# Optimization experiments

Hardware: AMD Instinct MI355X
Metric: run time of the kernel (lower is better)

Reference implementation:

```python
import jax, jax.numpy as jnp
import numpy as np

B, M, D, DE = 2, 256, 256, 64  # batch, tokens, in_dim, dep_embed_dim


def setup_inputs() -> dict:
    key = jax.random.key(0)
    ks = jax.random.split(key, 10)
    features = jax.random.normal(ks[0], (B, M + 1, D), jnp.float32)
    dep_type_adj = jax.random.normal(ks[1], (B, M, M, DE), jnp.float32)
    adj = (jax.random.uniform(ks[2], (B, M, M)) < 0.05).astype(jnp.int32)
    idx = jnp.arange(M)
    adj = adj.at[:, idx, idx].set(1)
    asp_start = jax.random.randint(ks[3], (B,), 0, 200, dtype=jnp.int32)
    asp_end = asp_start + 16
    s = lambda fan_in: 1.0 / np.sqrt(fan_in)
    Wz = jax.random.normal(ks[4], (D, D), jnp.float32) * s(D)
    bz = jax.random.normal(ks[5], (D,), jnp.float32) * s(D)
    Wa = jax.random.normal(ks[6], (D + DE + D,), jnp.float32) * s(D + DE + D)
    Wm = jax.random.normal(ks[7], (D, D + DE), jnp.float32) * s(D + DE)
    Wh = jax.random.normal(ks[8], (D, 2 * D), jnp.float32) * s(2 * D)
    return dict(features=features, dep_type_adj=dep_type_adj, deprel_adj=adj,
                asp_start=asp_start, asp_end=asp_end,
                Wz=Wz, bz=bz, Wa=Wa, Wm=Wm, Wh=Wh)


def reference(features, dep_type_adj, deprel_adj, asp_start, asp_end, Wz, bz, Wa, Wm, Wh):
    # z_linear
    zf = features @ Wz.T + bz                              # [B, M+1, D]
    f = zf[:, 1:]                                          # token feats [B, M, D]
    asp = zf[0, 1:]                                        # NOTE: original indexes features[0] (batch 0)

    # candidate neighbors for node i: out-edges (i,j) then in-edges (j,i) -> 2M slots
    dep_cat = jnp.concatenate([dep_type_adj, jnp.swapaxes(dep_type_adj, 1, 2)], axis=2)  # [B,M,2M,DE]
    mask = jnp.concatenate([deprel_adj, jnp.swapaxes(deprel_adj, 1, 2)], axis=2) != 0    # [B,M,2M]

    # attention_layer weight split over [dep | neighbor_feat | aspect_feat]
    wa_dep, wa_nf, wa_asp = Wa[:DE], Wa[DE:DE + D], Wa[DE + D:]
    s = (jnp.einsum('bike,e->bik', dep_cat, wa_dep)
         + jnp.tile(f @ wa_nf, (1, 2))[:, None, :]
         + (asp @ wa_asp)[None, :, None])                  # [B,M,2M]
    s = jnp.where(s > 0, s, 0.01 * s)                      # LeakyReLU(0.01)
    big_neg = jnp.finfo(s.dtype).min
    w = jax.nn.softmax(jnp.where(mask, s, big_neg), axis=-1)
    w = jnp.where(mask, w, 0.0)                            # edge-softmax over valid neighbors

    # w_m over [dep | neighbor_feat]
    Wm_dep, Wm_f = Wm[:, :DE], Wm[:, DE:]
    nf_proj = jnp.tile(f @ Wm_f.T, (1, 2, 1))              # [B,2M,D], neighbor part (i-independent)
    msg = jax.nn.relu(jnp.einsum('bike,de->bikd', dep_cat, Wm_dep) + nf_proj[:, None])  # [B,M,2M,D]
    fused = jnp.einsum('bik,bikd->bid', w, msg)            # weighted aggregate [B,M,D]

    # w_h over [fused | aspect]
    out_asp = jax.nn.relu(fused @ Wh[:, :D].T + (asp @ Wh[:, D:].T)[None])  # [B,M,D]

    # only aspect-span nodes are updated; +1 offset into the token axis
    pos = jnp.arange(M)
    upd = (pos[None, :] >= asp_start[:, None]) & (pos[None, :] < asp_end[:, None])  # [B,M]
    tokens = jnp.where(upd[..., None], out_asp, features[:, 1:])
    return jnp.concatenate([features[:, :1], tokens], axis=1)  # dropout is identity at inference
```

## Files before the change

### kernel.cpp

```cpp
#include <hip/hip_runtime.h>
#include <hip/hip_bf16.h>
#include <cstdint>

#define BB 2
#define MM 256
#define DD 256
#define DE 64
#define K2 (2*MM)
#define WM_LD (DD+DE)
#define WH_LD (2*DD)
#define DEP_LD 68

__device__ float4 g_Wz4   [64*DD];
__device__ float4 g_Wm4   [64*DD];
__device__ float4 g_WmDep4[16*DD];
__device__ float4 g_Wh4lo [64*DD];
__device__ float4 g_Wh4hi [64*DD];
__device__ float g_fproj [BB*MM*DD];
__device__ float g_fnf   [BB*MM];
__device__ float g_aspdot[MM];
__device__ float g_asph  [MM*DD];

__global__ __launch_bounds__(256) void k_tr(const float* __restrict__ Wz,
                                            const float* __restrict__ Wm,
                                            const float* __restrict__ Wh,
                                            const float4* __restrict__ src,
                                            float4* __restrict__ dst, int n4) {
  const int t = threadIdx.x, blk = blockIdx.x;
  const int c = t & 63, r0 = t >> 6;
  __shared__ float tile[64][65];

  const int gidx = blk*256 + t;
  if (gidx < n4) dst[gidx] = src[gidx];

  const float* s = nullptr; float4* d4 = nullptr;
  int ld = 0, row0 = 0, col0 = 0, e4base = 0;
  if (blk < 16)      { s = Wz; ld = DD;    row0 = (blk>>2)*64; col0 = (blk&3)*64;      d4 = g_Wz4;    e4base = (blk&3)*16; }
  else if (blk < 32) { int x = blk-16; s = Wm; ld = WM_LD; row0 = (x>>2)*64; col0 = DE + (x&3)*64; d4 = g_Wm4; e4base = (x&3)*16; }
  else if (blk < 36) { int x = blk-32; s = Wm; ld = WM_LD; row0 = x*64;      col0 = 0;             d4 = g_WmDep4; e4base = 0; }
  else if (blk < 68) { int x = blk-36; int rt = x>>3, cg = x&7; s = Wh; ld = WH_LD; row0 = rt*64; col0 = cg*64;
                       d4 = (cg < 4) ? g_Wh4lo : g_Wh4hi; e4base = (cg&3)*16; }
  if (s) {
    #pragma unroll
    for (int rr = r0; rr < 64; rr += 4)
      tile[rr][c] = s[(size_t)(row0 + rr)*ld + col0 + c];
    __syncthreads();
    #pragma unroll
    for (int je = r0; je < 16; je += 4)
      d4[(size_t)(e4base + je)*DD + row0 + c] =
        make_float4(tile[c][4*je+0], tile[c][4*je+1], tile[c][4*je+2], tile[c][4*je+3]);
  }
}

__global__ __launch_bounds__(256) void k_pre(const float* __restrict__ feats,
                                             const float* __restrict__ bz,
                                             const float* __restrict__ Wa,
                                             const int*   __restrict__ a_start,
                                             const int*   __restrict__ a_end) {
  const int blk = blockIdx.x;
  const int b   = blk >> 7;
  const int m0  = (blk & 127) * 2;
  const int t   = threadIdx.x;

  __shared__ float fin[2][DD];
  __shared__ float fzsh[2][DD];

  fin[0][t] = feats[((size_t)b*(MM+1) + m0 + 1)*DD + t];
  fin[1][t] = feats[((size_t)b*(MM+1) + m0 + 2)*DD + t];
  __syncthreads();

  float a0 = 0.f, a1 = 0.f;
  #pragma unroll 8
  for (int e4 = 0; e4 < 64; ++e4) {
    const float4 w  = g_Wz4[(size_t)e4*DD + t];
    const float4 f0 = *(const float4*)&fin[0][e4*4];
    const float4 f1 = *(const float4*)&fin[1][e4*4];
    a0 += f0.x*w.x + f0.y*w.y + f0.z*w.z + f0.w*w.w;
    a1 += f1.x*w.x + f1.y*w.y + f1.z*w.z + f1.w*w.w;
  }
  const float bzt = bz[t];
  fzsh[0][t] = a0 + bzt; fzsh[1][t] = a1 + bzt;
  __syncthreads();

  const int wv = t >> 6, lane = t & 63;
  const int s0 = a_start[0], e0 = a_end[0], s1 = a_start[1], e1 = a_end[1];
  if (wv < 2) {
    float p = 0.f;
    for (int e = lane; e < DD; e += 64) p += fzsh[wv][e] * Wa[DE + e];
    for (int off = 32; off > 0; off >>= 1) p += __shfl_down(p, off, 64);
    if (lane == 0) g_fnf[b*MM + m0 + wv] = p;
  } else if (b == 0) {
    const int rr = wv - 2;
    const int ri = m0 + rr;
    if ((ri >= s0 && ri < e0) || (ri >= s1 && ri < e1)) {
      float p = 0.f;
      for (int e = lane; e < DD; e += 64) p += fzsh[rr][e] * Wa[DE + DD + e];
      for (int off = 32; off > 0; off >>= 1) p += __shfl_down(p, off, 64);
      if (lane == 0) g_aspdot[ri] = p;
    }
  }

  float p0 = 0.f, p1 = 0.f;
  #pragma unroll 8
  for (int e4 = 0; e4 < 64; ++e4) {
    const float4 w  = g_Wm4[(size_t)e4*DD + t];
    const float4 f0 = *(const float4*)&fzsh[0][e4*4];
    const float4 f1 = *(const float4*)&fzsh[1][e4*4];
    p0 += f0.x*w.x + f0.y*w.y + f0.z*w.z + f0.w*w.w;
    p1 += f1.x*w.x + f1.y*w.y + f1.z*w.z + f1.w*w.w;
  }
  g_fproj[((size_t)b*MM + m0    )*DD + t] = p0;
  g_fproj[((size_t)b*MM + m0 + 1)*DD + t] = p1;

  if (b == 0) {
    const bool need0 = ((m0   >= s0 && m0   < e0) || (m0   >= s1 && m0   < e1));
    const bool need1 = ((m0+1 >= s0 && m0+1 < e0) || (m0+1 >= s1 && m0+1 < e1));
    if (need0 || need1) {
      float q0 = 0.f, q1 = 0.f;
      #pragma unroll 8
      for (int e4 = 0; e4 < 64; ++e4) {
        const float4 w  = g_Wh4hi[(size_t)e4*DD + t];
        const float4 f0 = *(const float4*)&fzsh[0][e4*4];
        const float4 f1 = *(const float4*)&fzsh[1][e4*4];
        q0 += f0.x*w.x + f0.y*w.y + f0.z*w.z + f0.w*w.w;
        q1 += f1.x*w.x + f1.y*w.y + f1.z*w.z + f1.w*w.w;
      }
      if (need0) g_asph[(size_t)(m0    )*DD + t] = q0;
      if (need1) g_asph[(size_t)(m0 + 1)*DD + t] = q1;
    }
  }
}

__global__ __launch_bounds__(256, 1) void k_attn(const float* __restrict__ dta,
                                                 const int*   __restrict__ adj,
                                                 const int*   __restrict__ a_start,
                                                 const int*   __restrict__ a_end,
                                                 const float* __restrict__ Wa,
                                                 float* __restrict__ out) {
  const int b = blockIdx.x >> 4;
  const int r = blockIdx.x & 15;
  const int i = a_start[b] + r;
  if (i >= a_end[b] || i >= MM) return;
  const int t = threadIdx.x;
  const int lane = t & 63, wv = t >> 6;
  const int d = t;

  __shared__ int   act[K2];
  __shared__ float sv [K2];
  __shared__ int   wcnt[8];
  __shared__ float wrm [4];
  __shared__ float wrs [4];
  __shared__ float wadep[DE];
  __shared__ float fnfsh[MM];
  __shared__ float depsh[64*DEP_LD];
  __shared__ float fproj_sh[64][DD];
  __shared__ float fused_sh[DD];

  const int mval0 = adj[((size_t)b*MM + i)*MM + t];
  const int mval1 = adj[((size_t)b*MM + t)*MM + i];
  float4 wm4[16];
  #pragma unroll
  for (int e4 = 0; e4 < 16; ++e4) wm4[e4] = g_WmDep4[(size_t)e4*DD + d];
  fnfsh[t] = g_fnf[b*MM + t];
  if (t < DE) wadep[t] = Wa[t];
  const float aspdot_i = g_aspdot[i];
  const float asph_i   = g_asph[(size_t)i*DD + d];

  const bool on0 = (mval0 != 0);
  const bool on1 = (mval1 != 0);
  const unsigned long long b0 = __ballot(on0);
  const unsigned long long b1 = __ballot(on1);
  if (lane == 0) { wcnt[wv] = __popcll(b0); wcnt[4+wv] = __popcll(b1); }
  __syncthreads();
  const int tot0 = wcnt[0] + wcnt[1] + wcnt[2] + wcnt[3];
  const int na   = tot0 + wcnt[4] + wcnt[5] + wcnt[6] + wcnt[7];
  {
    int off0 = 0, off1 = tot0;
    for (int w2 = 0; w2 < wv; ++w2) { off0 += wcnt[w2]; off1 += wcnt[4+w2]; }
    off0 += __popcll(b0 & ((1ull << lane) - 1ull));
    off1 += __popcll(b1 & ((1ull << lane) - 1ull));
    if (on0) act[off0] = t;
    if (on1) act[off1] = MM + t;
  }
  __syncthreads();

  const int cnt0 = (na < 64) ? na : 64;
  const int nq0  = cnt0 * 64;
  float4 stash[16];
  #pragma unroll
  for (int rr = 0; rr < 16; ++rr) {
    const int q = t + rr*256;
    if (q < nq0) {
      const int jl = q >> 6, c4 = q & 63;
      const int k = act[jl];
      stash[rr] = *((const float4*)(g_fproj + ((size_t)b*MM + (k & (MM-1)))*DD) + c4);
    }
  }

  const int jj = t >> 2, sub = t & 3;
  for (int base = 0; base < na; base += 64) {
    const int j = base + jj;
    float p = 0.f; int k = 0;
    if (j < na) {
      k = act[j];
      const float* dv = (k < MM) ? dta + (((size_t)b*MM + i)*MM + k)*DE
                                 : dta + (((size_t)b*MM + (k - MM))*MM + i)*DE;
      const float4* dv4 = (const float4*)dv + sub*4;
      const float4 v0 = dv4[0], v1 = dv4[1], v2 = dv4[2], v3 = dv4[3];
      const float* wa = wadep + sub*16;
      p = v0.x*wa[0]  + v0.y*wa[1]  + v0.z*wa[2]  + v0.w*wa[3]
        + v1.x*wa[4]  + v1.y*wa[5]  + v1.z*wa[6]  + v1.w*wa[7]
        + v2.x*wa[8]  + v2.y*wa[9]  + v2.z*wa[10] + v2.w*wa[11]
        + v3.x*wa[12] + v3.y*wa[13] + v3.z*wa[14] + v3.w*wa[15];
      if (base == 0) {
        float4* ds = (float4*)(depsh + jj*DEP_LD + sub*16);
        ds[0] = v0; ds[1] = v1; ds[2] = v2; ds[3] = v3;
      }
    }
    p += __shfl_xor(p, 1, 64);
    p += __shfl_xor(p, 2, 64);
    if (j < na && sub == 0) {
      const float s = p + fnfsh[k & (MM-1)] + aspdot_i;
      sv[j] = (s > 0.f) ? s : 0.01f * s;
    }
  }
  __syncthreads();

  {
    float part = -3.4e38f;
    for (int j = t; j < na; j += 256) part = fmaxf(part, sv[j]);
    for (int off = 32; off > 0; off >>= 1) part = fmaxf(part, __shfl_down(part, off, 64));
    if (lane == 0) wrm[wv] = part;
  }
  __syncthreads();
  const float mx = fmaxf(fmaxf(wrm[0], wrm[1]), fmaxf(wrm[2], wrm[3]));
  {
    float psum = 0.f;
    for (int j = t; j < na; j += 256) { float e = expf(sv[j] - mx); sv[j] = e; psum += e; }
    for (int off = 32; off > 0; off >>= 1) psum += __shfl_down(psum, off, 64);
    if (lane == 0) wrs[wv] = psum;
  }
  __syncthreads();
  const float inv = 1.f / (wrs[0] + wrs[1] + wrs[2] + wrs[3]);
  for (int j = t; j < na; j += 256) sv[j] *= inv;
  #pragma unroll
  for (int rr = 0; rr < 16; ++rr) {
    const int q = t + rr*256;
    if (q < nq0) { const int jl = q >> 6, c4 = q & 63; *(float4*)&fproj_sh[jl][c4*4] = stash[rr]; }
  }
  __syncthreads();

  float acc = 0.f;
  for (int base = 0; base < na; base += 64) {
    const int cnt = min(64, na - base);
    if (base > 0) {
      __syncthreads();
      for (int q = t; q < cnt*64; q += 256) {
        const int jl = q >> 6, c4 = q & 63;
        const int k = act[base + jl];
        *(float4*)&fproj_sh[jl][c4*4] =
          *((const float4*)(g_fproj + ((size_t)b*MM + (k & (MM-1)))*DD) + c4);
      }
      for (int q = t; q < cnt*16; q += 256) {
        const int jl = q >> 4, e4 = q & 15;
        const int k = act[base + jl];
        const float* dv = (k < MM) ? dta + (((size_t)b*MM + i)*MM + k)*DE
                                   : dta + (((size_t)b*MM + (k - MM))*MM + i)*DE;
        *(float4*)(depsh + jl*DEP_LD + e4*4) = ((const float4*)dv)[e4];
      }
      __syncthreads();
    }
    #pragma unroll 4
    for (int jl = 0; jl < cnt; ++jl) {
      const float4* dp = (const float4*)(depsh + jl*DEP_LD);
      float dot = 0.f;
      #pragma unroll
      for (int e4 = 0; e4 < 16; ++e4) {
        const float4 v = dp[e4];
        const float4 w = wm4[e4];
        dot += v.x*w.x + v.y*w.y + v.z*w.z + v.w*w.w;
      }
      float msg = dot + fproj_sh[jl][d];
      msg = (msg > 0.f) ? msg : 0.f;
      acc += sv[base + jl] * msg;
    }
  }
  fused_sh[d] = acc;
  __syncthreads();

  float o = asph_i;
  #pragma unroll 8
  for (int e4 = 0; e4 < 64; ++e4) {
    const float4 w = g_Wh4lo[(size_t)e4*DD + d];
    const float4 f = *(const float4*)&fused_sh[e4*4];
    o += f.x*w.x + f.y*w.y + f.z*w.z + f.w*w.w;
  }
  out[((size_t)b*(MM+1) + i + 1)*DD + d] = (o > 0.f) ? o : 0.f;
}

extern "C" void kernel_launch(void* const* d_in, const int* in_sizes, int n_in,
                              void* d_out, int out_size, void* d_ws, size_t ws_size,
                              hipStream_t stream) {
  const float* feats   = (const float*)d_in[0];
  const float* dta     = (const float*)d_in[1];
  const int*   adj     = (const int*)  d_in[2];
  const int*   a_start = (const int*)  d_in[3];
  const int*   a_end   = (const int*)  d_in[4];
  const float* Wz      = (const float*)d_in[5];
  const float* bz      = (const float*)d_in[6];
  const float* Wa      = (const float*)d_in[7];
  const float* Wm      = (const float*)d_in[8];
  const float* Wh      = (const float*)d_in[9];
  float* out = (float*)d_out;

  const int n4 = BB*(MM+1)*DD/4;
  k_tr  <<<132, 256, 0, stream>>>(Wz, Wm, Wh, (const float4*)feats, (float4*)out, n4);
  k_pre <<<BB*MM/2, 256, 0, stream>>>(feats, bz, Wa, a_start, a_end);
  k_attn<<<BB*16, 256, 0, stream>>>(dta, adj, a_start, a_end, Wa, out);
}
```

Baseline: 145.1 us.

## Fuse pre and attention kernels with atomic-counter handoff to overlap work

Merges the projection kernel and the attention kernel into one launch of 288 blocks. The first 32 blocks are attention blocks: they start the dependency-embedding attention dot products and then spin on a global counter until all 256 projection blocks have finished. This removes a kernel launch boundary and overlaps the dta reads with the projections. The shared fproj staging tile is dropped and fproj is now read directly from global memory per neighbor. The spin-wait depends on every projection block being scheduled alongside the waiting blocks, and the direct global reads may cost more than the old shared staging.

```diff
diff --git a/kernel.cpp b/kernel.cpp
--- a/kernel.cpp
+++ b/kernel.cpp
@@ -20,6 +20,7 @@
 __device__ float g_fnf   [BB*MM];
 __device__ float g_aspdot[MM];
 __device__ float g_asph  [MM*DD];
+__device__ int   g_done;
 
 __global__ __launch_bounds__(256) void k_tr(const float* __restrict__ Wz,
                                             const float* __restrict__ Wm,
@@ -27,6 +28,7 @@
                                             const float4* __restrict__ src,
                                             float4* __restrict__ dst, int n4) {
   const int t = threadIdx.x, blk = blockIdx.x;
+  if (blk == 0 && t == 0) g_done = 0;
   const int c = t & 63, r0 = t >> 6;
   __shared__ float tile[64][65];
 
@@ -52,202 +54,201 @@
   }
 }
 
-__global__ __launch_bounds__(256) void k_pre(const float* __restrict__ feats,
-                                             const float* __restrict__ bz,
-                                             const float* __restrict__ Wa,
-                                             const int*   __restrict__ a_start,
-                                             const int*   __restrict__ a_end) {
-  const int blk = blockIdx.x;
-  const int b   = blk >> 7;
-  const int m0  = (blk & 127) * 2;
-  const int t   = threadIdx.x;
-
-  __shared__ float fin[2][DD];
-  __shared__ float fzsh[2][DD];
-
-  fin[0][t] = feats[((size_t)b*(MM+1) + m0 + 1)*DD + t];
-  fin[1][t] = feats[((size_t)b*(MM+1) + m0 + 2)*DD + t];
-  __syncthreads();
-
-  float a0 = 0.f, a1 = 0.f;
-  #pragma unroll 8
-  for (int e4 = 0; e4 < 64; ++e4) {
-    const float4 w  = g_Wz4[(size_t)e4*DD + t];
-    const float4 f0 = *(const float4*)&fin[0][e4*4];
-    const float4 f1 = *(const float4*)&fin[1][e4*4];
-    a0 += f0.x*w.x + f0.y*w.y + f0.z*w.z + f0.w*w.w;
-    a1 += f1.x*w.x + f1.y*w.y + f1.z*w.z + f1.w*w.w;
-  }
-  const float bzt = bz[t];
-  fzsh[0][t] = a0 + bzt; fzsh[1][t] = a1 + bzt;
-  __syncthreads();
-
-  const int wv = t >> 6, lane = t & 63;
-  const int s0 = a_start[0], e0 = a_end[0], s1 = a_start[1], e1 = a_end[1];
-  if (wv < 2) {
-    float p = 0.f;
-    for (int e = lane; e < DD; e += 64) p += fzsh[wv][e] * Wa[DE + e];
-    for (int off = 32; off > 0; off >>= 1) p += __shfl_down(p, off, 64);
-    if (lane == 0) g_fnf[b*MM + m0 + wv] = p;
-  } else if (b == 0) {
-    const int rr = wv - 2;
-    const int ri = m0 + rr;
-    if ((ri >= s0 && ri < e0) || (ri >= s1 && ri < e1)) {
-      float p = 0.f;
-      for (int e = lane; e < DD; e += 64) p += fzsh[rr][e] * Wa[DE + DD + e];
-      for (int off = 32; off > 0; off >>= 1) p += __shfl_down(p, off, 64);
-      if (lane == 0) g_aspdot[ri] = p;
-    }
-  }
-
-  float p0 = 0.f, p1 = 0.f;
-  #pragma unroll 8
-  for (int e4 = 0; e4 < 64; ++e4) {
-    const float4 w  = g_Wm4[(size_t)e4*DD + t];
-    const float4 f0 = *(const float4*)&fzsh[0][e4*4];
-    const float4 f1 = *(const float4*)&fzsh[1][e4*4];
-    p0 += f0.x*w.x + f0.y*w.y + f0.z*w.z + f0.w*w.w;
-    p1 += f1.x*w.x + f1.y*w.y + f1.z*w.z + f1.w*w.w;
-  }
-  g_fproj[((size_t)b*MM + m0    )*DD + t] = p0;
-  g_fproj[((size_t)b*MM + m0 + 1)*DD + t] = p1;
-
-  if (b == 0) {
-    const bool need0 = ((m0   >= s0 && m0   < e0) || (m0   >= s1 && m0   < e1));
-    const bool need1 = ((m0+1 >= s0 && m0+1 < e0) || (m0+1 >= s1 && m0+1 < e1));
-    if (need0 || need1) {
-      float q0 = 0.f, q1 = 0.f;
-      #pragma unroll 8
-      for (int e4 = 0; e4 < 64; ++e4) {
-        const float4 w  = g_Wh4hi[(size_t)e4*DD + t];
-        const float4 f0 = *(const float4*)&fzsh[0][e4*4];
-        const float4 f1 = *(const float4*)&fzsh[1][e4*4];
-        q0 += f0.x*w.x + f0.y*w.y + f0.z*w.z + f0.w*w.w;
-        q1 += f1.x*w.x + f1.y*w.y + f1.z*w.z + f1.w*w.w;
-      }
-      if (need0) g_asph[(size_t)(m0    )*DD + t] = q0;
-      if (need1) g_asph[(size_t)(m0 + 1)*DD + t] = q1;
-    }
-  }
-}
-
-__global__ __launch_bounds__(256, 1) void k_attn(const float* __restrict__ dta,
-                                                 const int*   __restrict__ adj,
+struct PreSM  { float fin[2][DD]; float fzsh[2][DD]; };
+struct AttnSM {
+  int   act[K2];
+  float sv [K2];
+  int   wcnt[8];
+  float wrm[4], wrs[4];
+  float wadep[DE];
+  float fnfsh[MM];
+  float depsh[64*DEP_LD];
+  float fused_sh[DD];
+};
+union SMem { PreSM pre; AttnSM attn; };
+
+__global__ __launch_bounds__(256, 1) void k_main(const float* __restrict__ feats,
+                                                 const float* __restrict__ bz,
+                                                 const float* __restrict__ Wa,
                                                  const int*   __restrict__ a_start,
                                                  const int*   __restrict__ a_end,
-                                                 const float* __restrict__ Wa,
+                                                 const float* __restrict__ dta,
+                                                 const int*   __restrict__ adj,
                                                  float* __restrict__ out) {
-  const int b = blockIdx.x >> 4;
-  const int r = blockIdx.x & 15;
+  __shared__ SMem sm;
+  const int blk = blockIdx.x;
+  const int t = threadIdx.x;
+  const int lane = t & 63, wv = t >> 6;
+
+  if (blk >= 32) {
+    PreSM& P = sm.pre;
+    const int p  = blk - 32;
+    const int b  = p >> 7;
+    const int m0 = (p & 127) * 2;
+
+    P.fin[0][t] = feats[((size_t)b*(MM+1) + m0 + 1)*DD + t];
+    P.fin[1][t] = feats[((size_t)b*(MM+1) + m0 + 2)*DD + t];
+    __syncthreads();
+
+    float a0 = 0.f, a1 = 0.f;
+    #pragma unroll 8
+    for (int e4 = 0; e4 < 64; ++e4) {
+      const float4 w  = g_Wz4[(size_t)e4*DD + t];
+      const float4 f0 = *(const float4*)&P.fin[0][e4*4];
+      const float4 f1 = *(const float4*)&P.fin[1][e4*4];
+      a0 += f0.x*w.x + f0.y*w.y + f0.z*w.z + f0.w*w.w;
+      a1 += f1.x*w.x + f1.y*w.y + f1.z*w.z + f1.w*w.w;
+    }
+    const float bzt = bz[t];
+    P.fzsh[0][t] = a0 + bzt; P.fzsh[1][t] = a1 + bzt;
+    __syncthreads();
+
+    const int s0 = a_start[0], e0 = a_end[0], s1 = a_start[1], e1 = a_end[1];
+    if (wv < 2) {
+      float pp = 0.f;
+      for (int e = lane; e < DD; e += 64) pp += P.fzsh[wv][e] * Wa[DE + e];
+      for (int off = 32; off > 0; off >>= 1) pp += __shfl_down(pp, off, 64);
+      if (lane == 0) g_fnf[b*MM + m0 + wv] = pp;
+    } else if (b == 0) {
+      const int rr = wv - 2;
+      const int ri = m0 + rr;
+      if ((ri >= s0 && ri < e0) || (ri >= s1 && ri < e1)) {
+        float pp = 0.f;
+        for (int e = lane; e < DD; e += 64) pp += P.fzsh[rr][e] * Wa[DE + DD + e];
+        for (int off = 32; off > 0; off >>= 1) pp += __shfl_down(pp, off, 64);
+        if (lane == 0) g_aspdot[ri] = pp;
+      }
+    }
+
+    float p0 = 0.f, p1 = 0.f;
+    #pragma unroll 8
+    for (int e4 = 0; e4 < 64; ++e4) {
+      const float4 w  = g_Wm4[(size_t)e4*DD + t];
+      const float4 f0 = *(const float4*)&P.fzsh[0][e4*4];
+      const float4 f1 = *(const float4*)&P.fzsh[1][e4*4];
+      p0 += f0.x*w.x + f0.y*w.y + f0.z*w.z + f0.w*w.w;
+      p1 += f1.x*w.x + f1.y*w.y + f1.z*w.z + f1.w*w.w;
+    }
+    g_fproj[((size_t)b*MM + m0    )*DD + t] = p0;
+    g_fproj[((size_t)b*MM + m0 + 1)*DD + t] = p1;
+
+    if (b == 0) {
+      const bool need0 = ((m0   >= s0 && m0   < e0) || (m0   >= s1 && m0   < e1));
+      const bool need1 = ((m0+1 >= s0 && m0+1 < e0) || (m0+1 >= s1 && m0+1 < e1));
+      if (need0 || need1) {
+        float q0 = 0.f, q1 = 0.f;
+        #pragma unroll 8
+        for (int e4 = 0; e4 < 64; ++e4) {
+          const float4 w  = g_Wh4hi[(size_t)e4*DD + t];
+          const float4 f0 = *(const float4*)&P.fzsh[0][e4*4];
+          const float4 f1 = *(const float4*)&P.fzsh[1][e4*4];
+          q0 += f0.x*w.x + f0.y*w.y + f0.z*w.z + f0.w*w.w;
+          q1 += f1.x*w.x + f1.y*w.y + f1.z*w.z + f1.w*w.w;
+        }
+        if (need0) g_asph[(size_t)(m0    )*DD + t] = q0;
+        if (need1) g_asph[(size_t)(m0 + 1)*DD + t] = q1;
+      }
+    }
+
+    __syncthreads();
+    __threadfence();
+    if (t == 0)
+      __hip_atomic_fetch_add(&g_done, 1, __ATOMIC_RELEASE, __HIP_MEMORY_SCOPE_AGENT);
+    return;
+  }
+
+  AttnSM& A = sm.attn;
+  const int b = blk >> 4;
+  const int r = blk & 15;
   const int i = a_start[b] + r;
   if (i >= a_end[b] || i >= MM) return;
-  const int t = threadIdx.x;
-  const int lane = t & 63, wv = t >> 6;
   const int d = t;
-
-  __shared__ int   act[K2];
-  __shared__ float sv [K2];
-  __shared__ int   wcnt[8];
-  __shared__ float wrm [4];
-  __shared__ float wrs [4];
-  __shared__ float wadep[DE];
-  __shared__ float fnfsh[MM];
-  __shared__ float depsh[64*DEP_LD];
-  __shared__ float fproj_sh[64][DD];
-  __shared__ float fused_sh[DD];
 
   const int mval0 = adj[((size_t)b*MM + i)*MM + t];
   const int mval1 = adj[((size_t)b*MM + t)*MM + i];
   float4 wm4[16];
   #pragma unroll
   for (int e4 = 0; e4 < 16; ++e4) wm4[e4] = g_WmDep4[(size_t)e4*DD + d];
-  fnfsh[t] = g_fnf[b*MM + t];
-  if (t < DE) wadep[t] = Wa[t];
-  const float aspdot_i = g_aspdot[i];
-  const float asph_i   = g_asph[(size_t)i*DD + d];
+  if (t < DE) A.wadep[t] = Wa[t];
 
   const bool on0 = (mval0 != 0);
   const bool on1 = (mval1 != 0);
   const unsigned long long b0 = __ballot(on0);
   const unsigned long long b1 = __ballot(on1);
-  if (lane == 0) { wcnt[wv] = __popcll(b0); wcnt[4+wv] = __popcll(b1); }
-  __syncthreads();
-  const int tot0 = wcnt[0] + wcnt[1] + wcnt[2] + wcnt[3];
-  const int na   = tot0 + wcnt[4] + wcnt[5] + wcnt[6] + wcnt[7];
+  if (lane == 0) { A.wcnt[wv] = __popcll(b0); A.wcnt[4+wv] = __popcll(b1); }
+  __syncthreads();
+  const int tot0 = A.wcnt[0] + A.wcnt[1] + A.wcnt[2] + A.wcnt[3];
+  const int na   = tot0 + A.wcnt[4] + A.wcnt[5] + A.wcnt[6] + A.wcnt[7];
   {
     int off0 = 0, off1 = tot0;
-    for (int w2 = 0; w2 < wv; ++w2) { off0 += wcnt[w2]; off1 += wcnt[4+w2]; }
+    for (int w2 = 0; w2 < wv; ++w2) { off0 += A.wcnt[w2]; off1 += A.wcnt[4+w2]; }
     off0 += __popcll(b0 & ((1ull << lane) - 1ull));
     off1 += __popcll(b1 & ((1ull << lane) - 1ull));
-    if (on0) act[off0] = t;
-    if (on1) act[off1] = MM + t;
-  }
-  __syncthreads();
-
-  const int cnt0 = (na < 64) ? na : 64;
-  const int nq0  = cnt0 * 64;
-  float4 stash[16];
-  #pragma unroll
-  for (int rr = 0; rr < 16; ++rr) {
-    const int q = t + rr*256;
-    if (q < nq0) {
-      const int jl = q >> 6, c4 = q & 63;
-      const int k = act[jl];
-      stash[rr] = *((const float4*)(g_fproj + ((size_t)b*MM + (k & (MM-1)))*DD) + c4);
-    }
-  }
+    if (on0) A.act[off0] = t;
+    if (on1) A.act[off1] = MM + t;
+  }
+  __syncthreads();
 
   const int jj = t >> 2, sub = t & 3;
   for (int base = 0; base < na; base += 64) {
     const int j = base + jj;
-    float p = 0.f; int k = 0;
+    float p = 0.f;
     if (j < na) {
-      k = act[j];
+      const int k = A.act[j];
       const float* dv = (k < MM) ? dta + (((size_t)b*MM + i)*MM + k)*DE
                                  : dta + (((size_t)b*MM + (k - MM))*MM + i)*DE;
       const float4* dv4 = (const float4*)dv + sub*4;
       const float4 v0 = dv4[0], v1 = dv4[1], v2 = dv4[2], v3 = dv4[3];
-      const float* wa = wadep + sub*16;
+      const float* wa = A.wadep + sub*16;
       p = v0.x*wa[0]  + v0.y*wa[1]  + v0.z*wa[2]  + v0.w*wa[3]
         + v1.x*wa[4]  + v1.y*wa[5]  + v1.z*wa[6]  + v1.w*wa[7]
         + v2.x*wa[8]  + v2.y*wa[9]  + v2.z*wa[10] + v2.w*wa[11]
         + v3.x*wa[12] + v3.y*wa[13] + v3.z*wa[14] + v3.w*wa[15];
       if (base == 0) {
-        float4* ds = (float4*)(depsh + jj*DEP_LD + sub*16);
+        float4* ds = (float4*)(A.depsh + jj*DEP_LD + sub*16);
         ds[0] = v0; ds[1] = v1; ds[2] = v2; ds[3] = v3;
       }
     }
     p += __shfl_xor(p, 1, 64);
     p += __shfl_xor(p, 2, 64);
-    if (j < na && sub == 0) {
-      const float s = p + fnfsh[k & (MM-1)] + aspdot_i;
-      sv[j] = (s > 0.f) ? s : 0.01f * s;
-    }
+    if (j < na && sub == 0) A.sv[j] = p;
+  }
+
+  if (t == 0) {
+    while (__hip_atomic_load(&g_done, __ATOMIC_ACQUIRE, __HIP_MEMORY_SCOPE_AGENT) < 256) {
+      __builtin_amdgcn_s_sleep(16);
+    }
+  }
+  __syncthreads();
+
+  A.fnfsh[t] = g_fnf[b*MM + t];
+  const float aspdot_i = g_aspdot[i];
+  const float asph_i   = g_asph[(size_t)i*DD + d];
+  __syncthreads();
+
+  for (int j = t; j < na; j += 256) {
+    const float s = A.sv[j] + A.fnfsh[A.act[j] & (MM-1)] + aspdot_i;
+    A.sv[j] = (s > 0.f) ? s : 0.01f * s;
   }
   __syncthreads();
 
   {
     float part = -3.4e38f;
-    for (int j = t; j < na; j += 256) part = fmaxf(part, sv[j]);
+    for (int j = t; j < na; j += 256) part = fmaxf(part, A.sv[j]);
     for (int off = 32; off > 0; off >>= 1) part = fmaxf(part, __shfl_down(part, off, 64));
-    if (lane == 0) wrm[wv] = part;
-  }
-  __syncthreads();
-  const float mx = fmaxf(fmaxf(wrm[0], wrm[1]), fmaxf(wrm[2], wrm[3]));
+    if (lane == 0) A.wrm[wv] = part;
+  }
+  __syncthreads();
+  const float mx = fmaxf(fmaxf(A.wrm[0], A.wrm[1]), fmaxf(A.wrm[2], A.wrm[3]));
   {
     float psum = 0.f;
-    for (int j = t; j < na; j += 256) { float e = expf(sv[j] - mx); sv[j] = e; psum += e; }
+    for (int j = t; j < na; j += 256) { float e = expf(A.sv[j] - mx); A.sv[j] = e; psum += e; }
     for (int off = 32; off > 0; off >>= 1) psum += __shfl_down(psum, off, 64);
-    if (lane == 0) wrs[wv] = psum;
-  }
-  __syncthreads();
-  const float inv = 1.f / (wrs[0] + wrs[1] + wrs[2] + wrs[3]);
-  for (int j = t; j < na; j += 256) sv[j] *= inv;
-  #pragma unroll
-  for (int rr = 0; rr < 16; ++rr) {
-    const int q = t + rr*256;
-    if (q < nq0) { const int jl = q >> 6, c4 = q & 63; *(float4*)&fproj_sh[jl][c4*4] = stash[rr]; }
-  }
+    if (lane == 0) A.wrs[wv] = psum;
+  }
+  __syncthreads();
+  const float inv = 1.f / (A.wrs[0] + A.wrs[1] + A.wrs[2] + A.wrs[3]);
+  for (int j = t; j < na; j += 256) A.sv[j] *= inv;
   __syncthreads();
 
   float acc = 0.f;
@@ -255,24 +256,18 @@
     const int cnt = min(64, na - base);
     if (base > 0) {
       __syncthreads();
-      for (int q = t; q < cnt*64; q += 256) {
-        const int jl = q >> 6, c4 = q & 63;
-        const int k = act[base + jl];
-        *(float4*)&fproj_sh[jl][c4*4] =
-          *((const float4*)(g_fproj + ((size_t)b*MM + (k & (MM-1)))*DD) + c4);
-      }
       for (int q = t; q < cnt*16; q += 256) {
         const int jl = q >> 4, e4 = q & 15;
-        const int k = act[base + jl];
+        const int k = A.act[base + jl];
         const float* dv = (k < MM) ? dta + (((size_t)b*MM + i)*MM + k)*DE
                                    : dta + (((size_t)b*MM + (k - MM))*MM + i)*DE;
-        *(float4*)(depsh + jl*DEP_LD + e4*4) = ((const float4*)dv)[e4];
+        *(float4*)(A.depsh + jl*DEP_LD + e4*4) = ((const float4*)dv)[e4];
       }
       __syncthreads();
     }
     #pragma unroll 4
     for (int jl = 0; jl < cnt; ++jl) {
-      const float4* dp = (const float4*)(depsh + jl*DEP_LD);
+      const float4* dp = (const float4*)(A.depsh + jl*DEP_LD);
       float dot = 0.f;
       #pragma unroll
       for (int e4 = 0; e4 < 16; ++e4) {
@@ -280,19 +275,20 @@
         const float4 w = wm4[e4];
         dot += v.x*w.x + v.y*w.y + v.z*w.z + v.w*w.w;
       }
-      float msg = dot + fproj_sh[jl][d];
+      const int k = A.act[base + jl];
+      float msg = dot + g_fproj[((size_t)b*MM + (k & (MM-1)))*DD + d];
       msg = (msg > 0.f) ? msg : 0.f;
-      acc += sv[base + jl] * msg;
-    }
-  }
-  fused_sh[d] = acc;
+      acc += A.sv[base + jl] * msg;
+    }
+  }
+  A.fused_sh[d] = acc;
   __syncthreads();
 
   float o = asph_i;
   #pragma unroll 8
   for (int e4 = 0; e4 < 64; ++e4) {
     const float4 w = g_Wh4lo[(size_t)e4*DD + d];
-    const float4 f = *(const float4*)&fused_sh[e4*4];
+    const float4 f = *(const float4*)&A.fused_sh[e4*4];
     o += f.x*w.x + f.y*w.y + f.z*w.z + f.w*w.w;
   }
   out[((size_t)b*(MM+1) + i + 1)*DD + d] = (o > 0.f) ? o : 0.f;
@@ -315,6 +311,5 @@
 
   const int n4 = BB*(MM+1)*DD/4;
   k_tr  <<<132, 256, 0, stream>>>(Wz, Wm, Wh, (const float4*)feats, (float4*)out, n4);
-  k_pre <<<BB*MM/2, 256, 0, stream>>>(feats, bz, Wa, a_start, a_end);
-  k_attn<<<BB*16, 256, 0, stream>>>(dta, adj, a_start, a_end, Wa, out);
+  k_main<<<288, 256, 0, stream>>>(feats, bz, Wa, a_start, a_end, dta, adj, out);
 }
```

Measured after the change: 187.2 us. 29.0% more time.
